# Performance work log

Hardware: AMD Instinct MI355X
Metric: run time of the kernel (lower is better)

The kernel has to match this reference:

```python
import jax, jax.numpy as jnp
import numpy as np

B, S, D = 2, 2048, 1024
H, KS, VS = 16, 64, 64

def setup_inputs() -> dict:
    key = jax.random.key(0)
    ks = jax.random.split(key, 11)
    s = 1.0 / np.sqrt(D)
    return {
        "query": jax.random.normal(ks[0], (B, S, D), jnp.float32),
        "key":   jax.random.normal(ks[1], (B, S, D), jnp.float32),
        "value": jax.random.normal(ks[2], (B, S, D), jnp.float32),
        # weights stored [in, out] (transpose of torch Linear)
        "Wq": jax.random.normal(ks[3], (D, H * KS), jnp.float32) * s,
        "bq": jnp.zeros((H * KS,), jnp.float32),
        "Wk": jax.random.normal(ks[4], (D, H * KS), jnp.float32) * s,
        "bk": jnp.zeros((H * KS,), jnp.float32),
        "Wv": jax.random.normal(ks[5], (D, H * VS), jnp.float32) * s,
        "bv": jnp.zeros((H * VS,), jnp.float32),
        "Wo": jax.random.normal(ks[6], (H * VS, D), jnp.float32) * s,
        "bo": jnp.zeros((D,), jnp.float32),
    }

def reference(query, key, value, Wq, bq, Wk, bk, Wv, bv, Wo, bo):
    b = query.shape[0]
    # projections + split heads -> [B, H, S, d]
    Q = (query @ Wq + bq).reshape(b, -1, H, KS).transpose(0, 2, 1, 3)
    K = (key   @ Wk + bk).reshape(b, -1, H, KS).transpose(0, 2, 1, 3)
    V = (value @ Wv + bv).reshape(b, -1, H, VS).transpose(0, 2, 1, 3)
    scores = jnp.einsum('bhqd,bhkd->bhqk', Q, K) / jnp.sqrt(jnp.float32(KS))
    attn = jax.nn.softmax(scores, axis=-1)  # dropout_rate=0.0 -> identity
    ctx = jnp.einsum('bhqk,bhkd->bhqd', attn, V)  # [B,H,S,VS]
    ctx = ctx.transpose(0, 2, 1, 3).reshape(b, attn.shape[-1], H * VS)
    out = ctx @ Wo + bo
    return out, attn
```

## Files before the change

### kernel.cpp

```cpp
#include <hip/hip_runtime.h>
#include <stdint.h>


typedef _Float16 f16;
typedef f16 f16x4 __attribute__((ext_vector_type(4)));
typedef f16 f16x8 __attribute__((ext_vector_type(8)));
typedef float f32x4 __attribute__((ext_vector_type(4)));
typedef uint32_t u32;
typedef u32 u32x4 __attribute__((ext_vector_type(4)));

#define L2E 1.4426950408889634f

#define LDS_BARRIER() do { \
    asm volatile("s_waitcnt lgkmcnt(0)" ::: "memory"); \
    __builtin_amdgcn_sched_barrier(0); \
    __builtin_amdgcn_s_barrier(); \
} while (0)

__device__ __forceinline__ void gload16(const void* g, void* l) {
    __builtin_amdgcn_global_load_lds((__attribute__((address_space(1))) void*)g,
                                     (__attribute__((address_space(3))) void*)l,
                                     16, 0, 0);
}

__global__ __launch_bounds__(256) void k_cvt(const float* __restrict__ q,
                                             const float* __restrict__ k,
                                             const float* __restrict__ v,
                                             f16* __restrict__ dst)
{
    int z = blockIdx.z;
    const float* s = (z == 0) ? q : (z == 1) ? k : v;
    size_t i = (size_t)blockIdx.x * 256 + threadIdx.x;
    float4 f = ((const float4*)s)[i];
    f16x4 o = {(f16)f.x, (f16)f.y, (f16)f.z, (f16)f.w};
    *(f16x4*)(dst + (size_t)z * 4194304 + i * 4) = o;
}

__global__ __launch_bounds__(256) void k_wtrans(const float* __restrict__ w0,
                                                const float* __restrict__ w1,
                                                const float* __restrict__ w2,
                                                const float* __restrict__ w3,
                                                f16* __restrict__ wt)
{
    __shared__ f16 t[64][72];
    int z = blockIdx.z;
    const float* W = (z == 0) ? w0 : (z == 1) ? w1 : (z == 2) ? w2 : w3;
    f16* outp = wt + (size_t)z * 1048576;
    int tx = blockIdx.x, ty = blockIdx.y, tid = threadIdx.x;
#pragma unroll
    for (int r4 = 0; r4 < 4; r4++) {
        int row = r4 * 16 + (tid >> 4);
        int col = (tid & 15) * 4;
        float4 f = *(const float4*)(W + (size_t)(ty * 64 + row) * 1024 + tx * 64 + col);
        t[col + 0][row] = (f16)f.x; t[col + 1][row] = (f16)f.y;
        t[col + 2][row] = (f16)f.z; t[col + 3][row] = (f16)f.w;
    }
    __syncthreads();
#pragma unroll
    for (int cc = 0; cc < 2; cc++) {
        int c = tid + cc * 256;
        int row = c >> 3, ch = c & 7;
        f16x8 vv;
#pragma unroll
        for (int j = 0; j < 8; j++) vv[j] = t[row][ch * 8 + j];
        *(f16x8*)(outp + (size_t)(tx * 64 + row) * 1024 + ty * 64 + ch * 8) = vv;
    }
}

__global__ __launch_bounds__(256) void k_gemm(const f16* __restrict__ Ab,
                                              const f16* __restrict__ Wtb,
                                              const float* __restrict__ b0,
                                              const float* __restrict__ b1,
                                              const float* __restrict__ b2,
                                              void* __restrict__ o0,
                                              void* __restrict__ o1,
                                              int proj)
{
    __shared__ __align__(16) char As[16384];
    __shared__ __align__(16) char Bs[16384];
    const int tid = threadIdx.x;
    const int wv = tid >> 6, ln = tid & 63, lg = ln >> 4, li = ln & 15;
    const int m0 = blockIdx.y * 128, n0 = blockIdx.x * 128;
    const int wm = (wv >> 1) * 64, wn = (wv & 1) * 64;

    const f16* A; const f16* Bt; const float* bias; int mode;
    if (proj) {
        int z = blockIdx.z;
        A = Ab + (size_t)z * 4194304;
        Bt = Wtb + (size_t)z * 1048576;
        bias = (z == 0) ? b0 : (z == 1) ? b1 : b2;
        mode = (z == 2) ? 1 : 0;
    } else { A = Ab; Bt = Wtb; bias = b0; mode = 2; }

    const char* gA[4]; const char* gB[4];
#pragma unroll
    for (int c = 0; c < 4; c++) {
        int r = (wv * 4 + c) * 8 + (ln >> 3);
        int j = (ln & 7) ^ (r & 7);
        gA[c] = (const char*)A  + (size_t)(m0 + r) * 2048 + j * 16;
        gB[c] = (const char*)Bt + (size_t)(n0 + r) * 2048 + j * 16;
    }

    f32x4 acc[4][4] = {};
    for (int kt = 0; kt < 16; kt++) {
        __syncthreads();
#pragma unroll
        for (int c = 0; c < 4; c++) {
            gload16(gA[c] + kt * 128, As + (wv * 4 + c) * 1024);
            gload16(gB[c] + kt * 128, Bs + (wv * 4 + c) * 1024);
        }
        __syncthreads();
#pragma unroll
        for (int kk = 0; kk < 2; kk++) {
            f16x8 af[4], bf[4];
#pragma unroll
            for (int mi = 0; mi < 4; mi++) {
                int row = wm + mi * 16 + li;
                af[mi] = *(const f16x8*)(As + row * 128 + (((kk * 4 + lg) ^ (row & 7)) * 16));
            }
#pragma unroll
            for (int ni = 0; ni < 4; ni++) {
                int row = wn + ni * 16 + li;
                bf[ni] = *(const f16x8*)(Bs + row * 128 + (((kk * 4 + lg) ^ (row & 7)) * 16));
            }
#pragma unroll
            for (int mi = 0; mi < 4; mi++)
#pragma unroll
                for (int ni = 0; ni < 4; ni++)
                    acc[mi][ni] = __builtin_amdgcn_mfma_f32_16x16x32_f16(af[mi], bf[ni], acc[mi][ni], 0, 0, 0);
        }
    }

    float bvs[4];
#pragma unroll
    for (int ni = 0; ni < 4; ni++) bvs[ni] = bias[n0 + wn + ni * 16 + li];

    if (mode == 2) {
        float* O = (float*)o0;
#pragma unroll
        for (int mi = 0; mi < 4; mi++)
#pragma unroll
            for (int ni = 0; ni < 4; ni++) {
                int n = n0 + wn + ni * 16 + li;
#pragma unroll
                for (int r = 0; r < 4; r++) {
                    int m = m0 + wm + mi * 16 + lg * 4 + r;
                    O[(size_t)m * 1024 + n] = acc[mi][ni][r] + bvs[ni];
                }
            }
    } else if (mode == 0) {
        f16* O = (f16*)o0 + (size_t)blockIdx.z * 4194304;
#pragma unroll
        for (int mi = 0; mi < 4; mi++)
#pragma unroll
            for (int ni = 0; ni < 4; ni++) {
                int n = n0 + wn + ni * 16 + li;
                int h = n >> 6, d = n & 63;
#pragma unroll
                for (int r = 0; r < 4; r++) {
                    int m = m0 + wm + mi * 16 + lg * 4 + r;
                    int b = m >> 11, s = m & 2047;
                    O[(((size_t)b * 16 + h) * 2048 + s) * 64 + d] = (f16)(acc[mi][ni][r] + bvs[ni]);
                }
            }
    } else {
        f16* O = (f16*)o1;
#pragma unroll
        for (int mi = 0; mi < 4; mi++)
#pragma unroll
            for (int ni = 0; ni < 4; ni++) {
                int n = n0 + wn + ni * 16 + li;
                int h = n >> 6, d = n & 63;
                int mb = m0 + wm + mi * 16 + lg * 4;
                int b = mb >> 11, s = mb & 2047;
                f16x4 pk;
#pragma unroll
                for (int r = 0; r < 4; r++) pk[r] = (f16)(acc[mi][ni][r] + bvs[ni]);
                *(f16x4*)(O + (((size_t)b * 16 + h) * 64 + d) * 2048 + s) = pk;
            }
    }
}

__global__ __launch_bounds__(256, 3) void k_attn(const f16* __restrict__ Qb,
                                                 const f16* __restrict__ Kb,
                                                 const f16* __restrict__ Vt,
                                                 float* __restrict__ attn,
                                                 f16* __restrict__ ctx)
{
    __shared__ __align__(16) char Ks[16384];
    __shared__ __align__(16) char Ps[4][2048];
    const int tid = threadIdx.x, wv = tid >> 6, ln = tid & 63, lg = ln >> 4, li = ln & 15;
    const int bid = blockIdx.x;
    const int kk = bid >> 3;
    const int bh = (bid & 7) * 4 + (kk >> 5);
    const int q0 = (kk & 31) * 64 + wv * 16;

    const char* KbB = (const char*)Kb + (size_t)bh * 262144;
    const char* VtB = (const char*)Vt + (size_t)bh * 262144;

    const f16* qrow = Qb + ((size_t)bh * 2048 + q0 + li) * 64 + lg * 8;
    f16x8 aq0 = *(const f16x8*)(qrow);
    f16x8 aq1 = *(const f16x8*)(qrow + 32);
#pragma unroll
    for (int j = 0; j < 8; j++) {
        aq0[j] = (f16)((float)aq0[j] * 0.125f);
        aq1[j] = (f16)((float)aq1[j] * 0.125f);
    }

    const int r0 = tid >> 3, j0 = tid & 7;
    const int r1 = (tid + 256) >> 3, j1 = (tid + 256) & 7;
    const int sw0 = r0 * 128 + ((j0 ^ (r0 & 7)) * 16);
    const int sw1 = r1 * 128 + ((j1 ^ (r1 & 7)) * 16);

    float lacc[4] = {0.f, 0.f, 0.f, 0.f};
    {
        u32x4 sk0 = *(const u32x4*)(KbB + (size_t)r0 * 128 + j0 * 16);
        u32x4 sk1 = *(const u32x4*)(KbB + (size_t)r1 * 128 + j1 * 16);
        *(u32x4*)(Ks + sw0) = sk0;
        *(u32x4*)(Ks + sw1) = sk1;
        sk0 = *(const u32x4*)(KbB + (size_t)(64 + r0) * 128 + j0 * 16);
        sk1 = *(const u32x4*)(KbB + (size_t)(64 + r1) * 128 + j1 * 16);
        LDS_BARRIER();
        for (int kt = 0; kt < 32; kt++) {
            const char* cur = Ks + (kt & 1) * 8192;
            if (kt + 1 < 32) {
                char* nxt = Ks + ((kt + 1) & 1) * 8192;
                *(u32x4*)(nxt + sw0) = sk0;
                *(u32x4*)(nxt + sw1) = sk1;
                if (kt + 2 < 32) {
                    sk0 = *(const u32x4*)(KbB + (size_t)((kt + 2) * 64 + r0) * 128 + j0 * 16);
                    sk1 = *(const u32x4*)(KbB + (size_t)((kt + 2) * 64 + r1) * 128 + j1 * 16);
                }
            }
#pragma unroll
            for (int cf = 0; cf < 4; cf++) {
                int row = cf * 16 + li;
                f16x8 ak0 = *(const f16x8*)(cur + row * 128 + ((lg ^ (row & 7)) * 16));
                f16x8 ak1 = *(const f16x8*)(cur + row * 128 + (((4 + lg) ^ (row & 7)) * 16));
                __builtin_amdgcn_s_setprio(1);
                f32x4 z = {0.f, 0.f, 0.f, 0.f};
                z = __builtin_amdgcn_mfma_f32_16x16x32_f16(ak0, aq0, z, 0, 0, 0);
                z = __builtin_amdgcn_mfma_f32_16x16x32_f16(ak1, aq1, z, 0, 0, 0);
                __builtin_amdgcn_s_setprio(0);
                lacc[cf] += exp2f(z[0] * L2E) + exp2f(z[1] * L2E)
                          + exp2f(z[2] * L2E) + exp2f(z[3] * L2E);
            }
            if (kt + 1 < 32) LDS_BARRIER();
        }
    }
    float l_ = (lacc[0] + lacc[1]) + (lacc[2] + lacc[3]);
    l_ += __shfl_xor(l_, 16);
    l_ += __shfl_xor(l_, 32);
    const float llog = -log2f(l_);
    float* aRow = attn + ((size_t)bh * 2048 + q0 + li) * 2048;
    char* Pw = Ps[wv];

    f32x4 cacc[4] = {};

#define LOADV(buf, kt) do { \
    _Pragma("unroll") for (int df = 0; df < 4; df++) { \
        const char* vr = VtB + (size_t)(df * 16 + li) * 4096 + (kt) * 128 + lg * 16; \
        buf[df][0] = *(const f16x8*)vr; \
        buf[df][1] = *(const f16x8*)(vr + 64); \
    } } while (0)

#define STEP(kt, CUR, vbuf) do { \
    f32x4 zz[4]; \
    _Pragma("unroll") for (int cf = 0; cf < 4; cf++) { \
        int row = cf * 16 + li; \
        f16x8 ak0 = *(const f16x8*)((CUR) + row * 128 + ((lg ^ (row & 7)) * 16)); \
        f16x8 ak1 = *(const f16x8*)((CUR) + row * 128 + (((4 + lg) ^ (row & 7)) * 16)); \
        __builtin_amdgcn_s_setprio(1); \
        f32x4 z = {0.f, 0.f, 0.f, 0.f}; \
        z = __builtin_amdgcn_mfma_f32_16x16x32_f16(ak0, aq0, z, 0, 0, 0); \
        z = __builtin_amdgcn_mfma_f32_16x16x32_f16(ak1, aq1, z, 0, 0, 0); \
        __builtin_amdgcn_s_setprio(0); \
        zz[cf] = z; \
    } \
    _Pragma("unroll") for (int cf = 0; cf < 4; cf++) { \
        float p0 = exp2f(fmaf(zz[cf][0], L2E, llog)); \
        float p1 = exp2f(fmaf(zz[cf][1], L2E, llog)); \
        float p2 = exp2f(fmaf(zz[cf][2], L2E, llog)); \
        float p3 = exp2f(fmaf(zz[cf][3], L2E, llog)); \
        f32x4 fv = {p0, p1, p2, p3}; \
        __builtin_nontemporal_store(fv, (f32x4*)(aRow + (kt) * 64 + cf * 16 + lg * 4)); \
        f16x4 pk = {(f16)p0, (f16)p1, (f16)p2, (f16)p3}; \
        int c = cf * 2 + (lg >> 1); \
        *(f16x4*)(Pw + li * 128 + ((c ^ (li & 7)) * 16) + (lg & 1) * 8) = pk; \
    } \
    _Pragma("unroll") for (int s2 = 0; s2 < 2; s2++) { \
        f16x8 bp = *(const f16x8*)(Pw + li * 128 + (((s2 * 4 + lg) ^ (li & 7)) * 16)); \
        __builtin_amdgcn_s_setprio(1); \
        _Pragma("unroll") for (int df = 0; df < 4; df++) \
            cacc[df] = __builtin_amdgcn_mfma_f32_16x16x32_f16(vbuf[df][s2], bp, cacc[df], 0, 0, 0); \
        __builtin_amdgcn_s_setprio(0); \
    } } while (0)

    u32x4 sk0 = *(const u32x4*)(KbB + (size_t)r0 * 128 + j0 * 16);
    u32x4 sk1 = *(const u32x4*)(KbB + (size_t)r1 * 128 + j1 * 16);
    f16x8 vfA[4][2], vfB[4][2];
    LDS_BARRIER();
    *(u32x4*)(Ks + sw0) = sk0;
    *(u32x4*)(Ks + sw1) = sk1;
    sk0 = *(const u32x4*)(KbB + (size_t)(64 + r0) * 128 + j0 * 16);
    sk1 = *(const u32x4*)(KbB + (size_t)(64 + r1) * 128 + j1 * 16);
    LOADV(vfA, 0);
    LDS_BARRIER();

    for (int t = 0; t < 16; t++) {
        {
            char* nxt = Ks + 8192;
            *(u32x4*)(nxt + sw0) = sk0;
            *(u32x4*)(nxt + sw1) = sk1;
            if (t < 15) {
                sk0 = *(const u32x4*)(KbB + (size_t)((2 * t + 2) * 64 + r0) * 128 + j0 * 16);
                sk1 = *(const u32x4*)(KbB + (size_t)((2 * t + 2) * 64 + r1) * 128 + j1 * 16);
            }
            LOADV(vfB, 2 * t + 1);
            STEP(2 * t, Ks, vfA);
            LDS_BARRIER();
        }
        {
            if (t < 15) {
                *(u32x4*)(Ks + sw0) = sk0;
                *(u32x4*)(Ks + sw1) = sk1;
                sk0 = *(const u32x4*)(KbB + (size_t)((2 * t + 3) * 64 + r0) * 128 + j0 * 16);
                sk1 = *(const u32x4*)(KbB + (size_t)((2 * t + 3) * 64 + r1) * 128 + j1 * 16);
                LOADV(vfA, 2 * t + 2);
            }
            STEP(2 * t + 1, (const char*)(Ks + 8192), vfB);
            if (t < 15) LDS_BARRIER();
        }
    }
#undef LOADV
#undef STEP

    const int b = bh >> 4, h = bh & 15;
#pragma unroll
    for (int df = 0; df < 4; df++) {
        f16x4 pk;
#pragma unroll
        for (int r = 0; r < 4; r++) pk[r] = (f16)cacc[df][r];
        size_t mrow = (size_t)b * 2048 + q0 + li;
        size_t n = (size_t)h * 64 + df * 16 + lg * 4;
        *(f16x4*)(ctx + mrow * 1024 + n) = pk;
    }
}

extern "C" void kernel_launch(void* const* d_in, const int* in_sizes, int n_in,
                              void* d_out, int out_size, void* d_ws, size_t ws_size,
                              hipStream_t stream)
{
    const float* q  = (const float*)d_in[0];
    const float* k  = (const float*)d_in[1];
    const float* v  = (const float*)d_in[2];
    const float* Wq = (const float*)d_in[3];
    const float* bq = (const float*)d_in[4];
    const float* Wk = (const float*)d_in[5];
    const float* bk = (const float*)d_in[6];
    const float* Wv = (const float*)d_in[7];
    const float* bv = (const float*)d_in[8];
    const float* Wo = (const float*)d_in[9];
    const float* bo = (const float*)d_in[10];

    f16* W = (f16*)d_ws;
    float* out = (float*)d_out;
    float* attn = out + 4194304;

    f16* X   = W;
    f16* Wt  = W + 12582912;
    f16* QKb = W + 16777216;
    f16* Vt  = W + 25165824;
    f16* ctx = W + 29360128;

    k_cvt<<<dim3(4096, 1, 3), 256, 0, stream>>>(q, k, v, X);
    k_wtrans<<<dim3(16, 16, 4), 256, 0, stream>>>(Wq, Wk, Wv, Wo, Wt);
    k_gemm<<<dim3(8, 32, 3), 256, 0, stream>>>(X, Wt, bq, bk, bv, QKb, Vt, 1);
    k_attn<<<dim3(1024), 256, 0, stream>>>(QKb, QKb + 4194304, Vt, attn, ctx);
    k_gemm<<<dim3(8, 32, 1), 256, 0, stream>>>(ctx, Wt + 3145728, bo, bo, bo, out, nullptr, 0);
}
```

Measured before the change: 281.4 us.

## Split softmax row-sum pass into separate kernel with two query tiles per wave

Moves the first pass of the attention kernel, which computes the softmax denominators, into a new kernel. Each wave there handles 32 query rows instead of 16, so every K tile loaded into LDS is reused across twice as many queries. The attention kernel then reads the precomputed sums from workspace memory that the converted inputs used, which are no longer needed at that point. This adds a kernel launch and a small global round trip, and the new kernel runs at lower occupancy.

```diff
diff --git a/kernel.cpp b/kernel.cpp
--- a/kernel.cpp
+++ b/kernel.cpp
@@ -181,9 +181,88 @@
     }
 }
 
+__global__ __launch_bounds__(256, 2) void k_lsum(const f16* __restrict__ Qb,
+                                                 const f16* __restrict__ Kb,
+                                                 float* __restrict__ lout)
+{
+    __shared__ __align__(16) char Ks[16384];
+    const int tid = threadIdx.x, wv = tid >> 6, ln = tid & 63, lg = ln >> 4, li = ln & 15;
+    const int bid = blockIdx.x;
+    const int kk = bid >> 3;
+    const int bh = (bid & 7) * 4 + (kk >> 4);
+    const int q0 = (kk & 15) * 128 + wv * 32;
+
+    const char* KbB = (const char*)Kb + (size_t)bh * 262144;
+
+    f16x8 aq[2][2];
+#pragma unroll
+    for (int qf = 0; qf < 2; qf++) {
+        const f16* qrow = Qb + ((size_t)bh * 2048 + q0 + qf * 16 + li) * 64 + lg * 8;
+        aq[qf][0] = *(const f16x8*)(qrow);
+        aq[qf][1] = *(const f16x8*)(qrow + 32);
+#pragma unroll
+        for (int j = 0; j < 8; j++) {
+            aq[qf][0][j] = (f16)((float)aq[qf][0][j] * 0.125f);
+            aq[qf][1][j] = (f16)((float)aq[qf][1][j] * 0.125f);
+        }
+    }
+
+    const int r0 = tid >> 3, j0 = tid & 7;
+    const int r1 = (tid + 256) >> 3, j1 = (tid + 256) & 7;
+    const int sw0 = r0 * 128 + ((j0 ^ (r0 & 7)) * 16);
+    const int sw1 = r1 * 128 + ((j1 ^ (r1 & 7)) * 16);
+
+    float lacc[2][4] = {};
+    u32x4 sk0 = *(const u32x4*)(KbB + (size_t)r0 * 128 + j0 * 16);
+    u32x4 sk1 = *(const u32x4*)(KbB + (size_t)r1 * 128 + j1 * 16);
+    *(u32x4*)(Ks + sw0) = sk0;
+    *(u32x4*)(Ks + sw1) = sk1;
+    sk0 = *(const u32x4*)(KbB + (size_t)(64 + r0) * 128 + j0 * 16);
+    sk1 = *(const u32x4*)(KbB + (size_t)(64 + r1) * 128 + j1 * 16);
+    LDS_BARRIER();
+    for (int kt = 0; kt < 32; kt++) {
+        const char* cur = Ks + (kt & 1) * 8192;
+        if (kt + 1 < 32) {
+            char* nxt = Ks + ((kt + 1) & 1) * 8192;
+            *(u32x4*)(nxt + sw0) = sk0;
+            *(u32x4*)(nxt + sw1) = sk1;
+            if (kt + 2 < 32) {
+                sk0 = *(const u32x4*)(KbB + (size_t)((kt + 2) * 64 + r0) * 128 + j0 * 16);
+                sk1 = *(const u32x4*)(KbB + (size_t)((kt + 2) * 64 + r1) * 128 + j1 * 16);
+            }
+        }
+#pragma unroll
+        for (int cf = 0; cf < 4; cf++) {
+            int row = cf * 16 + li;
+            f16x8 ak0 = *(const f16x8*)(cur + row * 128 + ((lg ^ (row & 7)) * 16));
+            f16x8 ak1 = *(const f16x8*)(cur + row * 128 + (((4 + lg) ^ (row & 7)) * 16));
+            __builtin_amdgcn_s_setprio(1);
+            f32x4 z0 = {0.f, 0.f, 0.f, 0.f}, z1 = {0.f, 0.f, 0.f, 0.f};
+            z0 = __builtin_amdgcn_mfma_f32_16x16x32_f16(ak0, aq[0][0], z0, 0, 0, 0);
+            z0 = __builtin_amdgcn_mfma_f32_16x16x32_f16(ak1, aq[0][1], z0, 0, 0, 0);
+            z1 = __builtin_amdgcn_mfma_f32_16x16x32_f16(ak0, aq[1][0], z1, 0, 0, 0);
+            z1 = __builtin_amdgcn_mfma_f32_16x16x32_f16(ak1, aq[1][1], z1, 0, 0, 0);
+            __builtin_amdgcn_s_setprio(0);
+            lacc[0][cf] += exp2f(z0[0] * L2E) + exp2f(z0[1] * L2E)
+                         + exp2f(z0[2] * L2E) + exp2f(z0[3] * L2E);
+            lacc[1][cf] += exp2f(z1[0] * L2E) + exp2f(z1[1] * L2E)
+                         + exp2f(z1[2] * L2E) + exp2f(z1[3] * L2E);
+        }
+        if (kt + 1 < 32) LDS_BARRIER();
+    }
+#pragma unroll
+    for (int qf = 0; qf < 2; qf++) {
+        float l_ = (lacc[qf][0] + lacc[qf][1]) + (lacc[qf][2] + lacc[qf][3]);
+        l_ += __shfl_xor(l_, 16);
+        l_ += __shfl_xor(l_, 32);
+        if (lg == 0) lout[(size_t)bh * 2048 + q0 + qf * 16 + li] = l_;
+    }
+}
+
 __global__ __launch_bounds__(256, 3) void k_attn(const f16* __restrict__ Qb,
                                                  const f16* __restrict__ Kb,
                                                  const f16* __restrict__ Vt,
+                                                 const float* __restrict__ lsum,
                                                  float* __restrict__ attn,
                                                  f16* __restrict__ ctx)
 {
@@ -206,54 +285,14 @@
         aq0[j] = (f16)((float)aq0[j] * 0.125f);
         aq1[j] = (f16)((float)aq1[j] * 0.125f);
     }
+    const float llog = -log2f(lsum[(size_t)bh * 2048 + q0 + li]);
+    float* aRow = attn + ((size_t)bh * 2048 + q0 + li) * 2048;
+    char* Pw = Ps[wv];
 
     const int r0 = tid >> 3, j0 = tid & 7;
     const int r1 = (tid + 256) >> 3, j1 = (tid + 256) & 7;
     const int sw0 = r0 * 128 + ((j0 ^ (r0 & 7)) * 16);
     const int sw1 = r1 * 128 + ((j1 ^ (r1 & 7)) * 16);
-
-    float lacc[4] = {0.f, 0.f, 0.f, 0.f};
-    {
-        u32x4 sk0 = *(const u32x4*)(KbB + (size_t)r0 * 128 + j0 * 16);
-        u32x4 sk1 = *(const u32x4*)(KbB + (size_t)r1 * 128 + j1 * 16);
-        *(u32x4*)(Ks + sw0) = sk0;
-        *(u32x4*)(Ks + sw1) = sk1;
-        sk0 = *(const u32x4*)(KbB + (size_t)(64 + r0) * 128 + j0 * 16);
-        sk1 = *(const u32x4*)(KbB + (size_t)(64 + r1) * 128 + j1 * 16);
-        LDS_BARRIER();
-        for (int kt = 0; kt < 32; kt++) {
-            const char* cur = Ks + (kt & 1) * 8192;
-            if (kt + 1 < 32) {
-                char* nxt = Ks + ((kt + 1) & 1) * 8192;
-                *(u32x4*)(nxt + sw0) = sk0;
-                *(u32x4*)(nxt + sw1) = sk1;
-                if (kt + 2 < 32) {
-                    sk0 = *(const u32x4*)(KbB + (size_t)((kt + 2) * 64 + r0) * 128 + j0 * 16);
-                    sk1 = *(const u32x4*)(KbB + (size_t)((kt + 2) * 64 + r1) * 128 + j1 * 16);
-                }
-            }
-#pragma unroll
-            for (int cf = 0; cf < 4; cf++) {
-                int row = cf * 16 + li;
-                f16x8 ak0 = *(const f16x8*)(cur + row * 128 + ((lg ^ (row & 7)) * 16));
-                f16x8 ak1 = *(const f16x8*)(cur + row * 128 + (((4 + lg) ^ (row & 7)) * 16));
-                __builtin_amdgcn_s_setprio(1);
-                f32x4 z = {0.f, 0.f, 0.f, 0.f};
-                z = __builtin_amdgcn_mfma_f32_16x16x32_f16(ak0, aq0, z, 0, 0, 0);
-                z = __builtin_amdgcn_mfma_f32_16x16x32_f16(ak1, aq1, z, 0, 0, 0);
-                __builtin_amdgcn_s_setprio(0);
-                lacc[cf] += exp2f(z[0] * L2E) + exp2f(z[1] * L2E)
-                          + exp2f(z[2] * L2E) + exp2f(z[3] * L2E);
-            }
-            if (kt + 1 < 32) LDS_BARRIER();
-        }
-    }
-    float l_ = (lacc[0] + lacc[1]) + (lacc[2] + lacc[3]);
-    l_ += __shfl_xor(l_, 16);
-    l_ += __shfl_xor(l_, 32);
-    const float llog = -log2f(l_);
-    float* aRow = attn + ((size_t)bh * 2048 + q0 + li) * 2048;
-    char* Pw = Ps[wv];
 
     f32x4 cacc[4] = {};
 
@@ -299,7 +338,6 @@
     u32x4 sk0 = *(const u32x4*)(KbB + (size_t)r0 * 128 + j0 * 16);
     u32x4 sk1 = *(const u32x4*)(KbB + (size_t)r1 * 128 + j1 * 16);
     f16x8 vfA[4][2], vfB[4][2];
-    LDS_BARRIER();
     *(u32x4*)(Ks + sw0) = sk0;
     *(u32x4*)(Ks + sw1) = sk1;
     sk0 = *(const u32x4*)(KbB + (size_t)(64 + r0) * 128 + j0 * 16);
@@ -367,15 +405,17 @@
     float* out = (float*)d_out;
     float* attn = out + 4194304;
 
-    f16* X   = W;
-    f16* Wt  = W + 12582912;
-    f16* QKb = W + 16777216;
-    f16* Vt  = W + 25165824;
-    f16* ctx = W + 29360128;
+    f16* X    = W;
+    float* lsum = (float*)d_ws;
+    f16* Wt   = W + 12582912;
+    f16* QKb  = W + 16777216;
+    f16* Vt   = W + 25165824;
+    f16* ctx  = W + 29360128;
 
     k_cvt<<<dim3(4096, 1, 3), 256, 0, stream>>>(q, k, v, X);
     k_wtrans<<<dim3(16, 16, 4), 256, 0, stream>>>(Wq, Wk, Wv, Wo, Wt);
     k_gemm<<<dim3(8, 32, 3), 256, 0, stream>>>(X, Wt, bq, bk, bv, QKb, Vt, 1);
-    k_attn<<<dim3(1024), 256, 0, stream>>>(QKb, QKb + 4194304, Vt, attn, ctx);
+    k_lsum<<<dim3(512), 256, 0, stream>>>(QKb, QKb + 4194304, lsum);
+    k_attn<<<dim3(1024), 256, 0, stream>>>(QKb, QKb + 4194304, Vt, lsum, attn, ctx);
     k_gemm<<<dim3(8, 32, 1), 256, 0, stream>>>(ctx, Wt + 3145728, bo, bo, bo, out, nullptr, 0);
 }
```

Measured after the change: 299.3 us. +6.3%, slower.
